# Optimization experiments

Hardware: AMD Instinct MI355X
Metric: run time of the kernel (lower is better)

The kernel has to match this reference:

```python
import jax, jax.numpy as jnp
import numpy as np

D = 1024
N = 8192

def setup_inputs() -> dict:
    key = jax.random.key(0)
    ks = jax.random.split(key, 9)
    s = 1.0 / np.sqrt(D)
    return {
        "queries": jax.random.normal(ks[0], (N, D), dtype=jnp.float32),
        "key": jax.random.normal(ks[1], (N, D), dtype=jnp.float32),
        "values": jax.random.normal(ks[2], (N, D), dtype=jnp.float32),
        "Wq": jax.random.normal(ks[3], (D, D), dtype=jnp.float32) * s,
        "bq": jnp.zeros((D,), dtype=jnp.float32),
        "Wk": jax.random.normal(ks[4], (D, D), dtype=jnp.float32) * s,
        "bk": jnp.zeros((D,), dtype=jnp.float32),
        "Wv": jax.random.normal(ks[5], (D, D), dtype=jnp.float32) * s,
        "bv": jnp.zeros((D,), dtype=jnp.float32),
    }

def reference(queries, key, values, Wq, bq, Wk, bk, Wv, bv):
    # Linear layers: x @ W^T + b (torch nn.Linear convention)
    q = queries @ Wq.T + bq          # [N, D]
    k = key @ Wk.T + bk              # [N, D]
    v = values @ Wv.T + bv           # [N, D]
    scale = 1.0 / jnp.sqrt(jnp.asarray(float(q.shape[-1]), dtype=q.dtype))
    scores = (q @ k.T) * scale       # [N, N]
    p = jax.nn.softmax(scores, axis=-1)  # legacy nn.Softmax() on 2D -> dim=1
    return p @ v                     # [N, D]
```

## Files before the change

### kernel.cpp

```cpp
#include <hip/hip_runtime.h>
#include <hip/hip_bf16.h>
#include <stdint.h>

#define NN 8192
#define DD 1024

typedef __attribute__((ext_vector_type(4))) float f32x4;
typedef __attribute__((ext_vector_type(8))) short bf16x8;
using bf16_t = __hip_bfloat16;

__device__ __forceinline__ void gload16(const void* g, void* l) {
  __builtin_amdgcn_global_load_lds(
      (const __attribute__((address_space(1))) void*)g,
      (__attribute__((address_space(3))) void*)l, 16, 0, 0);
}
__device__ __forceinline__ int imin(int a, int b) { return a < b ? a : b; }

__global__ __launch_bounds__(256) void cast6_kernel(
    const float* __restrict__ i0, const float* __restrict__ i1,
    const float* __restrict__ i2, const float* __restrict__ w0,
    const float* __restrict__ w1, const float* __restrict__ w2,
    bf16_t* __restrict__ out_x, bf16_t* __restrict__ out_w) {
  const int nd8 = NN * DD / 8;
  const int dd8 = DD * DD / 8;
  int i = blockIdx.x * 256 + threadIdx.x;
  const float* src;
  bf16_t* dst;
  if (i < 3 * nd8) {
    const int r = i >> 20, j = i & (nd8 - 1);
    src = (r == 0 ? i0 : r == 1 ? i1 : i2) + (size_t)j * 8;
    dst = out_x + (size_t)i * 8;
  } else {
    const int k = i - 3 * nd8;
    const int r = k >> 17, j = k & (dd8 - 1);
    src = (r == 0 ? w0 : r == 1 ? w1 : w2) + (size_t)j * 8;
    dst = out_w + (size_t)k * 8;
  }
  const float4 a = ((const float4*)src)[0], b = ((const float4*)src)[1];
  __align__(16) bf16_t tmp[8];
  tmp[0] = __float2bfloat16(a.x); tmp[1] = __float2bfloat16(a.y);
  tmp[2] = __float2bfloat16(a.z); tmp[3] = __float2bfloat16(a.w);
  tmp[4] = __float2bfloat16(b.x); tmp[5] = __float2bfloat16(b.y);
  tmp[6] = __float2bfloat16(b.z); tmp[7] = __float2bfloat16(b.w);
  *(uint4*)dst = *(const uint4*)tmp;
}

__global__ __launch_bounds__(256, 2)
void gemm_proj(const bf16_t* __restrict__ Abase, const bf16_t* __restrict__ Wbase,
               const float* __restrict__ b0, const float* __restrict__ b1,
               const float* __restrict__ b2, bf16_t* __restrict__ C0,
               bf16_t* __restrict__ C1, bf16_t* __restrict__ C2) {
  __shared__ bf16_t As[128 * 32];
  __shared__ bf16_t Bs[128 * 32];
  const int y = blockIdx.y;
  const bf16_t* A = Abase + (size_t)y * NN * DD;
  const bf16_t* B = Wbase + (size_t)y * DD * DD;
  const float* bias = y == 0 ? b0 : y == 1 ? b1 : b2;
  bf16_t* C = y == 0 ? C0 : y == 1 ? C1 : C2;
  const float scale = y == 0 ? 0.03125f : 1.0f;
  const int ldc = y == 2 ? NN : DD;
  const int K = DD, nbx = DD / 128;

  const int t = threadIdx.x;
  const int nwg = gridDim.x;
  const int bid = (blockIdx.x & 7) * (nwg >> 3) + (blockIdx.x >> 3);
  const int bm = bid / nbx, bn = bid % nbx;
  const int lane = t & 63, wave = t >> 6;
  const int wr = wave >> 1, wc = wave & 1;

  const int c0 = t, c1 = t + 256;
  const bf16_t* ag0 = A + (size_t)(bm * 128 + (c0 >> 2)) * K + (c0 & 3) * 8;
  const bf16_t* ag1 = A + (size_t)(bm * 128 + (c1 >> 2)) * K + (c1 & 3) * 8;
  const bf16_t* bg0 = B + (size_t)(bn * 128 + (c0 >> 2)) * K + (c0 & 3) * 8;
  const bf16_t* bg1 = B + (size_t)(bn * 128 + (c1 >> 2)) * K + (c1 & 3) * 8;
  bf16_t* la0 = As + c0 * 8;
  bf16_t* la1 = As + c1 * 8;
  bf16_t* lb0 = Bs + c0 * 8;
  bf16_t* lb1 = Bs + c1 * 8;

  f32x4 acc[4][4] = {};
  const int fr = lane & 15;
  const int ko = (lane >> 4) * 8;

  for (int kt = 0; kt < K; kt += 32) {
    gload16(ag0 + kt, la0);
    gload16(ag1 + kt, la1);
    gload16(bg0 + kt, lb0);
    gload16(bg1 + kt, lb1);
    __syncthreads();
    bf16x8 af[4], bfv[4];
#pragma unroll
    for (int m = 0; m < 4; m++)
      af[m] = *(const bf16x8*)&As[(wr * 64 + m * 16 + fr) * 32 + ko];
#pragma unroll
    for (int n = 0; n < 4; n++)
      bfv[n] = *(const bf16x8*)&Bs[(wc * 64 + n * 16 + fr) * 32 + ko];
#pragma unroll
    for (int m = 0; m < 4; m++)
#pragma unroll
      for (int n = 0; n < 4; n++)
        acc[m][n] = __builtin_amdgcn_mfma_f32_16x16x32_bf16(af[m], bfv[n], acc[m][n], 0, 0, 0);
    __syncthreads();
  }

  const int rb = (lane >> 4) * 4;
#pragma unroll
  for (int m = 0; m < 4; m++) {
#pragma unroll
    for (int n = 0; n < 4; n++) {
      const int col = bn * 128 + wc * 64 + n * 16 + fr;
      const int row0 = bm * 128 + wr * 64 + m * 16 + rb;
      const float bv = bias[col];
      if (y != 2) {
#pragma unroll
        for (int j = 0; j < 4; j++)
          C[(size_t)(row0 + j) * ldc + col] = __float2bfloat16((acc[m][n][j] + bv) * scale);
      } else {
        __align__(8) bf16_t tmp[4];
#pragma unroll
        for (int j = 0; j < 4; j++)
          tmp[j] = __float2bfloat16(acc[m][n][j] + bv);
        *(ushort4*)&C[(size_t)col * ldc + row0] = *(const ushort4*)tmp;
      }
    }
  }
}

template<int MODE>
__global__ __launch_bounds__(512, 2)
void gemm256(const bf16_t* __restrict__ A, int lda,
             const bf16_t* __restrict__ B, int ldb,
             void* __restrict__ Cout, int ldc,
             float* __restrict__ aux, int ksplit, int nkt, int nbx, int Mrows) {
  __shared__ char smem_raw[131072];
  const int t = threadIdx.x;
  const int nwg = gridDim.x;
  const int bid = (blockIdx.x & 7) * (nwg >> 3) + (blockIdx.x >> 3);
  const int bm = bid / nbx, bn = bid % nbx;
  const int lane = t & 63, wave = t >> 6;
  const int wr = wave >> 2, wc = wave & 3;
  const int fr = lane & 15, hi = lane >> 4;
  const int k0 = blockIdx.y * ksplit;

  const int cswz = ((t & 7) ^ ((t >> 3) & 7)) * 8;
  uint32_t offA[2][2], offB[2][2];
#pragma unroll
  for (int h = 0; h < 2; h++)
#pragma unroll
    for (int l = 0; l < 2; l++) {
      const int r = h * 128 + l * 64 + (t >> 3);
      offA[h][l] = (uint32_t)((bm * 256 + r) * lda + k0 + cswz);
      offB[h][l] = (uint32_t)((bn * 256 + r) * ldb + k0 + cswz);
    }

  const int e = fr & 7;
  const int rowA = (wr * 128 + fr) * 128, rowB = (wc * 64 + fr) * 128;
  const int rdA_k0 = rowA + ((hi ^ e) << 4);
  const int rdA_k1 = rowA + (((hi + 4) ^ e) << 4);
  const int rdB_k0 = rowB + ((hi ^ e) << 4) + 32768;
  const int rdB_k1 = rowB + (((hi + 4) ^ e) << 4) + 32768;

  f32x4 acc[8][4] = {};
  bf16x8 af[4][2], bl[2][2], bh[2][2];

#define STA(buf, h, kt)                                                        \
  gload16(A + offA[h][0] + (size_t)(kt) * 64,                                  \
          smem_raw + (buf) * 65536 + (h) * 16384 + t * 16);                    \
  gload16(A + offA[h][1] + (size_t)(kt) * 64,                                  \
          smem_raw + (buf) * 65536 + (h) * 16384 + 8192 + t * 16);
#define STB(buf, h, kt)                                                        \
  gload16(B + offB[h][0] + (size_t)(kt) * 64,                                  \
          smem_raw + (buf) * 65536 + 32768 + (h) * 16384 + t * 16);            \
  gload16(B + offB[h][1] + (size_t)(kt) * 64,                                  \
          smem_raw + (buf) * 65536 + 32768 + (h) * 16384 + 8192 + t * 16);
#define RDA(buf, mf, ks)                                                       \
  (*(const bf16x8*)(smem_raw + (buf) * 65536 + ((ks) ? rdA_k1 : rdA_k0) +      \
                    (mf) * 2048))
#define RDB(buf, nf, ks)                                                       \
  (*(const bf16x8*)(smem_raw + (buf) * 65536 + ((ks) ? rdB_k1 : rdB_k0) +      \
                    (nf) * 2048))
#define MFMA8(BF, m0, n0)                                                      \
  _Pragma("unroll") for (int m = 0; m < 4; m++)                                \
  _Pragma("unroll") for (int n = 0; n < 2; n++)                                \
  _Pragma("unroll") for (int ks = 0; ks < 2; ks++)                             \
    acc[(m0) + m][(n0) + n] = __builtin_amdgcn_mfma_f32_16x16x32_bf16(         \
        af[m][ks], BF[n][ks], acc[(m0) + m][(n0) + n], 0, 0, 0);

  STB(0, 0, 0) STB(0, 1, 0) STA(0, 0, 0) STA(0, 1, 0)
  STB(1, 0, 1) STB(1, 1, 1)
  asm volatile("s_waitcnt vmcnt(4)" ::: "memory");
  __builtin_amdgcn_s_barrier();

  const int nit = nkt >> 1;
  for (int it = 0; it < nit; ++it) {
    const int T1 = 2 * it + 1;
    const int s2 = imin(2 * it + 2, nkt - 1);
    const int s3 = imin(2 * it + 3, nkt - 1);

#define TILEX(buf, S1, S2, S3, S4)                                             \
                                 \
    bl[0][0] = RDB(buf, 0, 0); bl[0][1] = RDB(buf, 0, 1);                      \
    bl[1][0] = RDB(buf, 1, 0); bl[1][1] = RDB(buf, 1, 1);                      \
    af[0][0] = RDA(buf, 0, 0); af[0][1] = RDA(buf, 0, 1);                      \
    af[1][0] = RDA(buf, 1, 0); af[1][1] = RDA(buf, 1, 1);                      \
    af[2][0] = RDA(buf, 2, 0); af[2][1] = RDA(buf, 2, 1);                      \
    af[3][0] = RDA(buf, 3, 0); af[3][1] = RDA(buf, 3, 1);                      \
    bh[0][0] = RDB(buf, 2, 0); bh[0][1] = RDB(buf, 2, 1);                      \
    bh[1][0] = RDB(buf, 3, 0); bh[1][1] = RDB(buf, 3, 1);                      \
    __builtin_amdgcn_s_setprio(1);                                             \
    MFMA8(bl, 0, 0)                                                            \
    MFMA8(bh, 0, 2)                                                            \
    __builtin_amdgcn_s_setprio(0);                                             \
                \
    __builtin_amdgcn_s_barrier();                                              \
    S1 S2 S3 S4                                                                \
    af[0][0] = RDA(buf, 4, 0); af[0][1] = RDA(buf, 4, 1);                      \
    af[1][0] = RDA(buf, 5, 0); af[1][1] = RDA(buf, 5, 1);                      \
    af[2][0] = RDA(buf, 6, 0); af[2][1] = RDA(buf, 6, 1);                      \
    af[3][0] = RDA(buf, 7, 0); af[3][1] = RDA(buf, 7, 1);                      \
    __builtin_amdgcn_s_setprio(1);                                             \
    MFMA8(bh, 4, 2)                                                            \
    MFMA8(bl, 4, 0)                                                            \
    __builtin_amdgcn_s_setprio(0);                                             \
    asm volatile("s_waitcnt vmcnt(4)" ::: "memory");                           \
    __builtin_amdgcn_s_barrier();

    TILEX(0, STA(1, 0, T1), STA(1, 1, T1), STB(0, 0, s2), STB(0, 1, s2))
    TILEX(1, STA(0, 0, s2), STA(0, 1, s2), STB(1, 0, s3), STB(1, 1, s3))
#undef TILEX
  }

  asm volatile("s_waitcnt vmcnt(0)" ::: "memory");
  __builtin_amdgcn_s_barrier();

  const int gr0 = bm * 256 + wr * 128 + hi * 4;
  const int gc0 = bn * 256 + wc * 64 + fr;

  if (MODE == 3) {
    float* rsum = (float*)smem_raw;
    if (t < 256) rsum[t] = 0.f;
    __syncthreads();
    bf16_t* C = (bf16_t*)Cout;
#pragma unroll
    for (int mf = 0; mf < 8; mf++) {
#pragma unroll
      for (int j = 0; j < 4; j++) {
        float rs = 0.f;
#pragma unroll
        for (int nf = 0; nf < 4; nf++) {
          float e2 = exp2f(acc[mf][nf][j] * 1.44269504088896f);
          bf16_t pb = __float2bfloat16(e2);
          C[(size_t)(gr0 + mf * 16 + j) * ldc + gc0 + nf * 16] = pb;
          rs += __bfloat162float(pb);
        }
        rs += __shfl_xor(rs, 1); rs += __shfl_xor(rs, 2);
        rs += __shfl_xor(rs, 4); rs += __shfl_xor(rs, 8);
        if (fr == 0) atomicAdd(&rsum[wr * 128 + mf * 16 + hi * 4 + j], rs);
      }
    }
    __syncthreads();
    if (t < 256) aux[(size_t)bn * Mrows + bm * 256 + t] = rsum[t];
  } else {
    float* C = (float*)Cout;
#pragma unroll
    for (int mf = 0; mf < 8; mf++)
#pragma unroll
      for (int j = 0; j < 4; j++) {
        const int row = gr0 + mf * 16 + j;
        const float s = aux[row];
#pragma unroll
        for (int nf = 0; nf < 4; nf++)
          atomicAdd(&C[(size_t)row * ldc + gc0 + nf * 16], acc[mf][nf][j] * s);
      }
  }
#undef STA
#undef STB
#undef RDA
#undef RDB
#undef MFMA8
}

__global__ __launch_bounds__(256) void rowsum_inv_kernel(
    const float* __restrict__ partial, float* __restrict__ inv_l, int nb) {
  const int r = blockIdx.x * 256 + threadIdx.x;
  float s = 0.f;
  for (int b = 0; b < nb; b++) s += partial[(size_t)b * NN + r];
  inv_l[r] = 1.f / s;
}

__global__ __launch_bounds__(256) void zero_kernel(float4* __restrict__ p) {
  p[(size_t)blockIdx.x * 256 + threadIdx.x] = make_float4(0.f, 0.f, 0.f, 0.f);
}

extern "C" void kernel_launch(void* const* d_in, const int* in_sizes, int n_in,
                              void* d_out, int out_size, void* d_ws, size_t ws_size,
                              hipStream_t stream) {
  const float* queries = (const float*)d_in[0];
  const float* key_in  = (const float*)d_in[1];
  const float* values  = (const float*)d_in[2];
  const float* Wq = (const float*)d_in[3];
  const float* bq = (const float*)d_in[4];
  const float* Wk = (const float*)d_in[5];
  const float* bk = (const float*)d_in[6];
  const float* Wv = (const float*)d_in[7];
  const float* bv = (const float*)d_in[8];
  float* out = (float*)d_out;
  char* ws = (char*)d_ws;

  const size_t MB = 1024 * 1024;
  bf16_t* qb = (bf16_t*)(ws);
  bf16_t* kb = (bf16_t*)(ws + 16 * MB);
  bf16_t* vT = (bf16_t*)(ws + 32 * MB);
  bf16_t* P  = (bf16_t*)(ws + 48 * MB);
  float* partial = (float*)(ws + 176 * MB);
  float* inv_l   = (float*)(ws + 177 * MB);
  bf16_t* x3 = (bf16_t*)(ws + 48 * MB);
  bf16_t* w3 = (bf16_t*)(ws + 96 * MB);

  const int nd8 = NN * DD / 8, dd8 = DD * DD / 8;

  cast6_kernel<<<(3 * nd8 + 3 * dd8) / 256, 256, 0, stream>>>(
      queries, key_in, values, Wq, Wk, Wv, x3, w3);
  gemm_proj<<<dim3((NN / 128) * (DD / 128), 3), 256, 0, stream>>>(
      x3, w3, bq, bk, bv, qb, kb, vT);
  gemm256<3><<<dim3((NN / 256) * (NN / 256)), 512, 0, stream>>>(
      qb, DD, kb, DD, P, NN, partial, 0, DD / 64, NN / 256, NN);
  rowsum_inv_kernel<<<NN / 256, 256, 0, stream>>>(partial, inv_l, NN / 256);
  zero_kernel<<<NN * DD / 4 / 256, 256, 0, stream>>>((float4*)out);
  gemm256<4><<<dim3((NN / 256) * (DD / 256), 2), 512, 0, stream>>>(
      P, NN, vT, NN, out, DD, inv_l, NN / 2, NN / 2 / 64, DD / 256, NN);
}
```

Before: 401.4 us.

## Fuse fp32-to-bf16 activation cast into projection GEMM loads

Removes the separate cast pass over the three N×D fp32 activation inputs. The projection GEMM now loads fp32 tiles directly into LDS and converts them to bf16 while building fragments. Both the A and B LDS tiles use XOR-swizzled layouts to avoid bank conflicts. This saves writing and re-reading about 48MB of bf16 intermediates, at the cost of double the LDS traffic and capacity for A and extra conversion instructions inside the K loop.

```diff
diff --git a/kernel.cpp b/kernel.cpp
--- a/kernel.cpp
+++ b/kernel.cpp
@@ -16,85 +16,97 @@
 }
 __device__ __forceinline__ int imin(int a, int b) { return a < b ? a : b; }
 
-__global__ __launch_bounds__(256) void cast6_kernel(
-    const float* __restrict__ i0, const float* __restrict__ i1,
-    const float* __restrict__ i2, const float* __restrict__ w0,
-    const float* __restrict__ w1, const float* __restrict__ w2,
-    bf16_t* __restrict__ out_x, bf16_t* __restrict__ out_w) {
-  const int nd8 = NN * DD / 8;
-  const int dd8 = DD * DD / 8;
-  int i = blockIdx.x * 256 + threadIdx.x;
-  const float* src;
-  bf16_t* dst;
-  if (i < 3 * nd8) {
-    const int r = i >> 20, j = i & (nd8 - 1);
-    src = (r == 0 ? i0 : r == 1 ? i1 : i2) + (size_t)j * 8;
-    dst = out_x + (size_t)i * 8;
-  } else {
-    const int k = i - 3 * nd8;
-    const int r = k >> 17, j = k & (dd8 - 1);
-    src = (r == 0 ? w0 : r == 1 ? w1 : w2) + (size_t)j * 8;
-    dst = out_w + (size_t)k * 8;
-  }
+__global__ __launch_bounds__(256) void cast_w_kernel(
+    const float* __restrict__ w0, const float* __restrict__ w1,
+    const float* __restrict__ w2, bf16_t* __restrict__ out_w) {
+  const int i = blockIdx.x * 256 + threadIdx.x;
+  const int r = i >> 17, j = i & ((1 << 17) - 1);
+  const float* src = (r == 0 ? w0 : r == 1 ? w1 : w2) + (size_t)j * 8;
   const float4 a = ((const float4*)src)[0], b = ((const float4*)src)[1];
   __align__(16) bf16_t tmp[8];
   tmp[0] = __float2bfloat16(a.x); tmp[1] = __float2bfloat16(a.y);
   tmp[2] = __float2bfloat16(a.z); tmp[3] = __float2bfloat16(a.w);
   tmp[4] = __float2bfloat16(b.x); tmp[5] = __float2bfloat16(b.y);
   tmp[6] = __float2bfloat16(b.z); tmp[7] = __float2bfloat16(b.w);
-  *(uint4*)dst = *(const uint4*)tmp;
+  *((uint4*)out_w + i) = *(const uint4*)tmp;
 }
 
 __global__ __launch_bounds__(256, 2)
-void gemm_proj(const bf16_t* __restrict__ Abase, const bf16_t* __restrict__ Wbase,
+void gemm_proj(const float* __restrict__ xq, const float* __restrict__ xk,
+               const float* __restrict__ xv, const bf16_t* __restrict__ Wbase,
                const float* __restrict__ b0, const float* __restrict__ b1,
                const float* __restrict__ b2, bf16_t* __restrict__ C0,
                bf16_t* __restrict__ C1, bf16_t* __restrict__ C2) {
-  __shared__ bf16_t As[128 * 32];
+  __shared__ float Asf[128 * 32];
   __shared__ bf16_t Bs[128 * 32];
   const int y = blockIdx.y;
-  const bf16_t* A = Abase + (size_t)y * NN * DD;
-  const bf16_t* B = Wbase + (size_t)y * DD * DD;
+  const float* X = y == 0 ? xq : y == 1 ? xk : xv;
+  const bf16_t* W = Wbase + (size_t)y * DD * DD;
   const float* bias = y == 0 ? b0 : y == 1 ? b1 : b2;
   bf16_t* C = y == 0 ? C0 : y == 1 ? C1 : C2;
   const float scale = y == 0 ? 0.03125f : 1.0f;
   const int ldc = y == 2 ? NN : DD;
-  const int K = DD, nbx = DD / 128;
 
   const int t = threadIdx.x;
   const int nwg = gridDim.x;
   const int bid = (blockIdx.x & 7) * (nwg >> 3) + (blockIdx.x >> 3);
-  const int bm = bid / nbx, bn = bid % nbx;
+  const int bm = bid >> 3, bn = bid & 7;
   const int lane = t & 63, wave = t >> 6;
   const int wr = wave >> 1, wc = wave & 1;
-
-  const int c0 = t, c1 = t + 256;
-  const bf16_t* ag0 = A + (size_t)(bm * 128 + (c0 >> 2)) * K + (c0 & 3) * 8;
-  const bf16_t* ag1 = A + (size_t)(bm * 128 + (c1 >> 2)) * K + (c1 & 3) * 8;
-  const bf16_t* bg0 = B + (size_t)(bn * 128 + (c0 >> 2)) * K + (c0 & 3) * 8;
-  const bf16_t* bg1 = B + (size_t)(bn * 128 + (c1 >> 2)) * K + (c1 & 3) * 8;
-  bf16_t* la0 = As + c0 * 8;
-  bf16_t* la1 = As + c1 * 8;
-  bf16_t* lb0 = Bs + c0 * 8;
-  bf16_t* lb1 = Bs + c1 * 8;
+  const int fr = lane & 15, hi = lane >> 4;
+
+  uint32_t aoff[4];
+  float* adst[4];
+#pragma unroll
+  for (int j = 0; j < 4; j++) {
+    const int c = t + j * 256;
+    const int row = c >> 3, l = (c & 7) ^ (row & 7);
+    aoff[j] = (uint32_t)((bm * 128 + row) * DD + l * 4);
+    adst[j] = Asf + c * 4;
+  }
+  uint32_t boff[2];
+  bf16_t* bdst[2];
+#pragma unroll
+  for (int j = 0; j < 2; j++) {
+    const int c = t + j * 256;
+    const int line = c >> 3, sp = (c & 7) ^ (line & 7);
+    const int row = line * 2 + (sp & 1), kc = sp >> 1;
+    boff[j] = (uint32_t)((bn * 128 + row) * DD + kc * 8);
+    bdst[j] = Bs + c * 8;
+  }
 
   f32x4 acc[4][4] = {};
-  const int fr = lane & 15;
-  const int ko = (lane >> 4) * 8;
-
-  for (int kt = 0; kt < K; kt += 32) {
-    gload16(ag0 + kt, la0);
-    gload16(ag1 + kt, la1);
-    gload16(bg0 + kt, lb0);
-    gload16(bg1 + kt, lb1);
+  const int e = fr & 7;
+
+  for (int kt = 0; kt < DD; kt += 32) {
+    gload16(X + aoff[0] + kt, adst[0]);
+    gload16(X + aoff[1] + kt, adst[1]);
+    gload16(X + aoff[2] + kt, adst[2]);
+    gload16(X + aoff[3] + kt, adst[3]);
+    gload16(W + boff[0] + kt, bdst[0]);
+    gload16(W + boff[1] + kt, bdst[1]);
     __syncthreads();
     bf16x8 af[4], bfv[4];
 #pragma unroll
-    for (int m = 0; m < 4; m++)
-      af[m] = *(const bf16x8*)&As[(wr * 64 + m * 16 + fr) * 32 + ko];
-#pragma unroll
-    for (int n = 0; n < 4; n++)
-      bfv[n] = *(const bf16x8*)&Bs[(wc * 64 + n * 16 + fr) * 32 + ko];
+    for (int m = 0; m < 4; m++) {
+      const int row = wr * 64 + m * 16 + fr;
+      const f32x4 v0 = *(const f32x4*)&Asf[row * 32 + (((2 * hi) ^ e) << 2)];
+      const f32x4 v1 = *(const f32x4*)&Asf[row * 32 + (((2 * hi + 1) ^ e) << 2)];
+      __align__(16) bf16_t tmp[8];
+#pragma unroll
+      for (int j2 = 0; j2 < 4; j2++) {
+        tmp[j2] = __float2bfloat16(v0[j2]);
+        tmp[4 + j2] = __float2bfloat16(v1[j2]);
+      }
+      af[m] = *(const bf16x8*)tmp;
+    }
+#pragma unroll
+    for (int n = 0; n < 4; n++) {
+      const int row = wc * 64 + n * 16 + fr;
+      const int line = row >> 1;
+      const int slot = (2 * hi + (row & 1)) ^ (line & 7);
+      bfv[n] = *(const bf16x8*)((const char*)Bs + line * 128 + slot * 16);
+    }
 #pragma unroll
     for (int m = 0; m < 4; m++)
 #pragma unroll
@@ -103,7 +115,7 @@
     __syncthreads();
   }
 
-  const int rb = (lane >> 4) * 4;
+  const int rb = hi * 4;
 #pragma unroll
   for (int m = 0; m < 4; m++) {
 #pragma unroll
@@ -198,7 +210,6 @@
     const int s3 = imin(2 * it + 3, nkt - 1);
 
 #define TILEX(buf, S1, S2, S3, S4)                                             \
-                                 \
     bl[0][0] = RDB(buf, 0, 0); bl[0][1] = RDB(buf, 0, 1);                      \
     bl[1][0] = RDB(buf, 1, 0); bl[1][1] = RDB(buf, 1, 1);                      \
     af[0][0] = RDA(buf, 0, 0); af[0][1] = RDA(buf, 0, 1);                      \
@@ -211,7 +222,6 @@
     MFMA8(bl, 0, 0)                                                            \
     MFMA8(bh, 0, 2)                                                            \
     __builtin_amdgcn_s_setprio(0);                                             \
-                \
     __builtin_amdgcn_s_barrier();                                              \
     S1 S2 S3 S4                                                                \
     af[0][0] = RDA(buf, 4, 0); af[0][1] = RDA(buf, 4, 1);                      \
@@ -314,15 +324,13 @@
   bf16_t* P  = (bf16_t*)(ws + 48 * MB);
   float* partial = (float*)(ws + 176 * MB);
   float* inv_l   = (float*)(ws + 177 * MB);
-  bf16_t* x3 = (bf16_t*)(ws + 48 * MB);
-  bf16_t* w3 = (bf16_t*)(ws + 96 * MB);
-
-  const int nd8 = NN * DD / 8, dd8 = DD * DD / 8;
-
-  cast6_kernel<<<(3 * nd8 + 3 * dd8) / 256, 256, 0, stream>>>(
-      queries, key_in, values, Wq, Wk, Wv, x3, w3);
+  bf16_t* w3 = (bf16_t*)(ws + 48 * MB);
+
+  const int dd8 = DD * DD / 8;
+
+  cast_w_kernel<<<3 * dd8 / 256, 256, 0, stream>>>(Wq, Wk, Wv, w3);
   gemm_proj<<<dim3((NN / 128) * (DD / 128), 3), 256, 0, stream>>>(
-      x3, w3, bq, bk, bv, qb, kb, vT);
+      queries, key_in, values, w3, bq, bk, bv, qb, kb, vT);
   gemm256<3><<<dim3((NN / 256) * (NN / 256)), 512, 0, stream>>>(
       qb, DD, kb, DD, P, NN, partial, 0, DD / 64, NN / 256, NN);
   rowsum_inv_kernel<<<NN / 256, 256, 0, stream>>>(partial, inv_l, NN / 256);
```

Result: slower. 417.2 us (+3.9%).
